# Performance work log

Measured on AMD Instinct MI355X. Metric: run time of the kernel, lower is better.

Reference implementation:

```python
import jax, jax.numpy as jnp
import numpy as np

BN_EPS = 1e-5


def _deconv_block(x, w, gamma, beta, mean, var):
    # Keras Conv2DTranspose(k=4, s=2, padding='valid') + Cropping2D(1) == pad (1,1) transpose conv: doubles H,W.
    y = jax.lax.conv_transpose(x, w, strides=(2, 2), padding=((1, 1), (1, 1)),
                               dimension_numbers=('NHWC', 'HWIO', 'NHWC'))
    # inference-mode BatchNorm followed by ReLU
    y = gamma * (y - mean) * jax.lax.rsqrt(var + BN_EPS) + beta
    return jax.nn.relu(y)


def _heatmap_max_det(hm):
    # hm: [B, H, W, K] (channels_last). Vectorized version of HeatmapMaxDetBlock.
    B, H, W, K = hm.shape
    flat = jnp.transpose(hm.reshape(B, H * W, K), (0, 2, 1))  # [B, K, HW]
    idx = jnp.argmax(flat, axis=2)                            # [B, K] int
    scores = jnp.max(flat, axis=2)                            # [B, K]
    pos = scores > 0.0                                        # scores_mask
    px = jnp.where(pos, (idx % W).astype(jnp.int32), 0)       # masked integer coords
    py = jnp.where(pos, (idx // W).astype(jnp.int32), 0)
    inner = (px > 0) & (px < W - 1) & (py > 0) & (py < H - 1)
    base = py * W + px

    def g(off):
        i = jnp.clip(base + off, 0, H * W - 1)                # clip keeps gathers in-bounds; masked by `inner`
        return jnp.take_along_axis(flat, i[..., None], axis=2)[..., 0]

    dx = jnp.where(inner, jnp.sign(g(1) - g(-1)) * 0.25, 0.0)   # subpixel refine in x
    dy = jnp.where(inner, jnp.sign(g(W) - g(-W)) * 0.25, 0.0)   # subpixel refine in y
    pts_x = px.astype(hm.dtype) + dx
    pts_y = py.astype(hm.dtype) + dy
    return jnp.stack([pts_x, pts_y, scores], axis=-1)            # [B, K, 3]


def setup_inputs() -> dict:
    key = jax.random.key(0)
    ks = jax.random.split(key, 24)
    B, Hf, Wf, Cb = 64, 8, 6, 2048
    C, KPT = 256, 17
    d = {}
    d['x'] = jax.random.normal(ks[0], (B, Hf, Wf, Cb), jnp.float32)
    ins = [Cb, C, C]
    for i in range(3):
        j = 1 + 6 * i
        d[f'w{i+1}'] = jax.random.normal(ks[j], (4, 4, ins[i], C), jnp.float32) * 0.05
        d[f'g{i+1}'] = jnp.ones((C,), jnp.float32) + 0.1 * jax.random.normal(ks[j + 1], (C,), jnp.float32)
        d[f'b{i+1}'] = 0.1 * jax.random.normal(ks[j + 2], (C,), jnp.float32)
        d[f'm{i+1}'] = 0.1 * jax.random.normal(ks[j + 3], (C,), jnp.float32)
        d[f'v{i+1}'] = 0.5 + jax.random.uniform(ks[j + 4], (C,), jnp.float32)
    d['wf'] = jax.random.normal(ks[20], (C, KPT), jnp.float32) * 0.05
    d['bf'] = 0.01 * jax.random.normal(ks[21], (KPT,), jnp.float32)
    return d


def reference(x, w1, g1, b1, m1, v1, w2, g2, b2, m2, v2, w3, g3, b3, m3, v3, wf, bf):
    y = _deconv_block(x, w1, g1, b1, m1, v1)   # [B,16,12,256]
    y = _deconv_block(y, w2, g2, b2, m2, v2)   # [B,32,24,256]
    y = _deconv_block(y, w3, g3, b3, m3, v3)   # [B,64,48,256]
    heatmap = jnp.einsum('bhwc,ck->bhwk', y, wf) + bf  # conv1x1 final block, [B,64,48,17]
    return _heatmap_max_det(heatmap)           # [B,17,3] (x, y, score)
```

## Files before the change

### kernel.cpp

```cpp
#include <hip/hip_runtime.h>


#define BN_EPS 1e-5f

typedef __attribute__((ext_vector_type(8))) short short8;
typedef __attribute__((ext_vector_type(4))) short short4v;
typedef __attribute__((ext_vector_type(4))) float float4v;
typedef unsigned int uint;

__device__ __forceinline__ float4v mfma16(short8 a, short8 b, float4v c) {
  return __builtin_amdgcn_mfma_f32_16x16x32_bf16(a, b, c, 0, 0, 0);
}

__device__ __forceinline__ void bf16split(float v, short& h, short& l) {
  const uint u  = __float_as_uint(v);
  const uint hb = (u + 0x7FFFu + ((u >> 16) & 1u)) >> 16;
  const float hf = __uint_as_float(hb << 16);
  const float lo = v - hf;
  const uint ul = __float_as_uint(lo);
  const uint lb = (ul + 0x7FFFu + ((ul >> 16) & 1u)) >> 16;
  h = (short)hb; l = (short)lb;
}

__device__ __forceinline__ uint pack2(short h0, short h1) {
  return (uint)(unsigned short)h0 | ((uint)(unsigned short)h1 << 16);
}

template <int CIN>
__global__ __launch_bounds__(256) void convert_w(
    const float* __restrict__ wg, short* __restrict__ wh, short* __restrict__ wl)
{
  constexpr int NCH = CIN / 32;
  __shared__ float tile[32][33];
  const int tap = blockIdx.x, ch = blockIdx.y, cb2 = blockIdx.z;
  const int tid = threadIdx.x;
#pragma unroll
  for (int k = 0; k < 4; ++k) {
    const int idx = k * 256 + tid;
    const int ci_l = idx >> 5, co_l = idx & 31;
    tile[ci_l][co_l] =
        wg[((size_t)(tap * CIN) + ch * 32 + ci_l) * 256 + cb2 * 32 + co_l];
  }
  __syncthreads();
#pragma unroll
  for (int k = 0; k < 2; ++k) {
    const int dd = k * 256 + tid;
    const int f = dd >> 8, wd = dd & 255;
    const int lane = wd >> 2, jp = (wd & 3) * 2;
    const int quad = lane >> 4, lrow = lane & 15;
    const int ci_l = quad * 8 + jp, co_l = f * 16 + lrow;
    short h0, l0, h1, l1;
    bf16split(tile[ci_l][co_l], h0, l0);
    bf16split(tile[ci_l + 1][co_l], h1, l1);
    const size_t off = ((size_t)((tap * NCH + ch) * 16 + cb2 * 2 + f)) * 512 +
                       lane * 8 + jp;
    *(uint*)(wh + off) = pack2(h0, h1);
    *(uint*)(wl + off) = pack2(l0, l1);
  }
}

__global__ __launch_bounds__(256) void convert_wf(
    const float* __restrict__ wf, short* __restrict__ wh, short* __restrict__ wl)
{
  const int b = blockIdx.x;
  const int ch = b >> 1, cb = b & 1;
  const int t = threadIdx.x;
  const int lane = t >> 2, jp = (t & 3) * 2;
  const int quad = lane >> 4, lrow = lane & 15;
  const int ci = ch * 32 + quad * 8 + jp;
  const int co = cb * 16 + lrow;
  const float v0 = (co < 17) ? wf[ci * 17 + co] : 0.f;
  const float v1 = (co < 17) ? wf[(ci + 1) * 17 + co] : 0.f;
  short h0, l0, h1, l1;
  bf16split(v0, h0, l0); bf16split(v1, h1, l1);
  const size_t off = (size_t)b * 512 + lane * 8 + jp;
  *(uint*)(wh + off) = pack2(h0, h1);
  *(uint*)(wl + off) = pack2(l0, l1);
}

template <int CIN, int H_IN, int W_IN, int MT, bool FUSE>
__global__ __launch_bounds__(256, 2) void deconv_mfma(
    const short* __restrict__ yh, const short* __restrict__ yl,
    const short* __restrict__ wbh, const short* __restrict__ wbl,
    const float* __restrict__ gg, const float* __restrict__ bg,
    const float* __restrict__ mg, const float* __restrict__ vg,
    float* __restrict__ og,
    short* __restrict__ oh_, short* __restrict__ ol_,
    const short* __restrict__ wfh, const short* __restrict__ wfl,
    const float* __restrict__ bfg)
{
  constexpr int R = H_IN - 1, C = W_IN - 1, NPIX = R * C;
  constexpr int H_OUT = 2 * H_IN - 2, W_OUT = 2 * W_IN - 2;
  constexpr int MF = MT / 16;
  constexpr int NCH = CIN / 32;
  constexpr int OUTSPAN = (MT + C - 2) / C + 1;
  constexpr int RSPAN = OUTSPAN + 1;
  constexpr int CIP = 40;
  constexpr int POS = RSPAN * W_IN;
  constexpr int AN = POS * CIP;
  constexpr int NITEM = POS * 16;
  constexpr int NIT = (NITEM + 255) / 256;
  constexpr int YSP = 264;

  __shared__ __align__(16) short ah_s[2][AN];
  __shared__ __align__(16) short al_s[2][AN];
  __shared__ __align__(16) short ysh_s[FUSE ? 32 * YSP : 1];
  __shared__ __align__(16) short ysl_s[FUSE ? 32 * YSP : 1];

  const int tid = threadIdx.x;
  const int wid = tid >> 6, lane = tid & 63;
  const int quad = lane >> 4, lrow = lane & 15;
  const int n0 = wid << 6;
  const int p = (int)(blockIdx.y >> 1), q = (int)(blockIdx.y & 1);
  const int n = blockIdx.z;

  int tapid[4];
#pragma unroll
  for (int t = 0; t < 4; ++t)
    tapid[t] = ((1 - p + 2 * (t >> 1)) << 2) + (1 - q + 2 * (t & 1));

  const int p0 = (int)blockIdx.x * MT;
  const int r_base = p0 / C;

  int abase[MF];
#pragma unroll
  for (int mf = 0; mf < MF; ++mf) {
    int pidx = p0 + mf * 16 + lrow;
    if (pidx > NPIX - 1) pidx = NPIX - 1;
    const int r = pidx / C, c = pidx % C;
    abase[mf] = ((r - r_base) * W_IN + c) * CIP + (quad << 3);
  }

  const int s_half = (tid >> 3) & 1;
  const short* __restrict__ gsrc = s_half ? yl : yh;
  int s_goff[NIT], s_loff[NIT];
#pragma unroll
  for (int k = 0; k < NIT; ++k) {
    const int i = k * 256 + tid;
    const int pos = i >> 4, sub = i & 7;
    const int row = pos / W_IN, col = pos - row * W_IN;
    int ih = r_base + row;
    if (ih > H_IN - 1) ih = H_IN - 1;
    s_goff[k] = ((n * H_IN + ih) * W_IN + col) * CIN + sub * 4;
    s_loff[k] = pos * CIP + sub * 4;
  }

  float4v acc[MF][4];
#pragma unroll
  for (int mf = 0; mf < MF; ++mf)
#pragma unroll
    for (int nf = 0; nf < 4; ++nf) acc[mf][nf] = (float4v){0.f, 0.f, 0.f, 0.f};

  short4v rv[NIT];
#pragma unroll
  for (int k = 0; k < NIT; ++k)
    if (NITEM % 256 == 0 || k * 256 + tid < NITEM)
      rv[k] = *(const short4v*)(gsrc + s_goff[k]);
  {
    short* lb = s_half ? &al_s[0][0] : &ah_s[0][0];
#pragma unroll
    for (int k = 0; k < NIT; ++k)
      if (NITEM % 256 == 0 || k * 256 + tid < NITEM)
        *(short4v*)(lb + s_loff[k]) = rv[k];
  }
  __syncthreads();

#pragma unroll 1
  for (int ck = 0; ck < NCH; ++ck) {
    const int b = ck & 1;
    const bool pre = (ck + 1 < NCH);
    if (pre) {
      const int ci0 = (ck + 1) * 32;
#pragma unroll
      for (int k = 0; k < NIT; ++k)
        if (NITEM % 256 == 0 || k * 256 + tid < NITEM)
          rv[k] = *(const short4v*)(gsrc + s_goff[k] + ci0);
    }
    const short* ab  = &ah_s[b][0];
    const short* alp = &al_s[b][0];
#pragma unroll
    for (int t = 0; t < 4; ++t) {
      short8 Bh[4], Bl[4];
#pragma unroll
      for (int nf = 0; nf < 4; ++nf) {
        const size_t fo =
            ((size_t)((tapid[t] * NCH + ck) * 16 + (wid << 2) + nf)) * 512 + lane * 8;
        Bh[nf] = *(const short8*)(wbh + fo);
        Bl[nf] = *(const short8*)(wbl + fo);
      }
      const int toff = ((t >> 1) * W_IN + (t & 1)) * CIP;
#pragma unroll
      for (int mf = 0; mf < MF; ++mf) {
        const short8 Ah = *(const short8*)(ab + abase[mf] + toff);
        const short8 Al = *(const short8*)(alp + abase[mf] + toff);
#pragma unroll
        for (int nf = 0; nf < 4; ++nf) {
          acc[mf][nf] = mfma16(Ah, Bh[nf], acc[mf][nf]);
          acc[mf][nf] = mfma16(Ah, Bl[nf], acc[mf][nf]);
          acc[mf][nf] = mfma16(Al, Bh[nf], acc[mf][nf]);
        }
      }
    }
    if (pre) {
      short* lb = s_half ? &al_s[b ^ 1][0] : &ah_s[b ^ 1][0];
#pragma unroll
      for (int k = 0; k < NIT; ++k)
        if (NITEM % 256 == 0 || k * 256 + tid < NITEM)
          *(short4v*)(lb + s_loff[k]) = rv[k];
    }
    __syncthreads();
  }

  float scv[4], shv[4];
#pragma unroll
  for (int nf = 0; nf < 4; ++nf) {
    const int co = n0 + nf * 16 + lrow;
    const float sc = gg[co] * rsqrtf(vg[co] + BN_EPS);
    scv[nf] = sc; shv[nf] = bg[co] - mg[co] * sc;
  }

  if constexpr (!FUSE) {
#pragma unroll
    for (int mf = 0; mf < MF; ++mf)
#pragma unroll
      for (int reg = 0; reg < 4; ++reg) {
        const int pidx = p0 + mf * 16 + (quad << 2) + reg;
        if (pidx < NPIX) {
          const int r = pidx / C, c = pidx % C;
          const int oh = 2 * r + p, ow = 2 * c + q;
          const size_t base =
              ((size_t)(n * H_OUT + oh) * W_OUT + ow) * 256 + n0 + lrow;
#pragma unroll
          for (int nf = 0; nf < 4; ++nf) {
            const float v = fmaxf(0.f, fmaf(acc[mf][nf][reg], scv[nf], shv[nf]));
            short h, l; bf16split(v, h, l);
            oh_[base + nf * 16] = h;
            ol_[base + nf * 16] = l;
          }
        }
      }
  } else {
    constexpr int NSUB = MT / 32;
    const int co_out = (wid << 4) + lrow;
#pragma unroll
    for (int s = 0; s < NSUB; ++s) {
      __syncthreads();
#pragma unroll
      for (int mh = 0; mh < 2; ++mh) {
        const int mf = 2 * s + mh;
        const int pl = (mh << 4) + (quad << 2);
#pragma unroll
        for (int reg = 0; reg < 4; ++reg)
#pragma unroll
          for (int nf = 0; nf < 4; ++nf) {
            const float v = fmaxf(0.f, fmaf(acc[mf][nf][reg], scv[nf], shv[nf]));
            short h, l; bf16split(v, h, l);
            const int o = (pl + reg) * YSP + n0 + nf * 16 + lrow;
            ysh_s[o] = h; ysl_s[o] = l;
          }
      }
      __syncthreads();
      if (wid < 2) {
        float4v hacc[2];
        hacc[0] = (float4v){0.f, 0.f, 0.f, 0.f};
        hacc[1] = (float4v){0.f, 0.f, 0.f, 0.f};
#pragma unroll
        for (int ch = 0; ch < 8; ++ch) {
          const size_t bo = (size_t)(ch * 2 + wid) * 512 + lane * 8;
          const short8 Hh = *(const short8*)(wfh + bo);
          const short8 Hl = *(const short8*)(wfl + bo);
#pragma unroll
          for (int mh = 0; mh < 2; ++mh) {
            const int yo = (mh * 16 + lrow) * YSP + (ch << 5) + (quad << 3);
            const short8 Ah = *(const short8*)(ysh_s + yo);
            const short8 Al = *(const short8*)(ysl_s + yo);
            hacc[mh] = mfma16(Ah, Hh, hacc[mh]);
            hacc[mh] = mfma16(Ah, Hl, hacc[mh]);
            hacc[mh] = mfma16(Al, Hh, hacc[mh]);
          }
        }
        if (co_out < 17) {
          const float bias = bfg[co_out];
#pragma unroll
          for (int mh = 0; mh < 2; ++mh)
#pragma unroll
            for (int reg = 0; reg < 4; ++reg) {
              const int pidx = p0 + s * 32 + mh * 16 + (quad << 2) + reg;
              if (pidx < NPIX) {
                const int r = pidx / C, c = pidx % C;
                const int oh = 2 * r + p, ow = 2 * c + q;
                og[((size_t)(n * H_OUT + oh) * W_OUT + ow) * 17 + co_out] =
                    hacc[mh][reg] + bias;
              }
            }
        }
      }
    }
  }
}

template <int MT, int KS>
__global__ __launch_bounds__(256, 2) void deconv1_mfma(
    const float* __restrict__ xg,
    const short* __restrict__ wbh, const short* __restrict__ wbl,
    float* __restrict__ og)
{
  constexpr int CIN = 2048, NCH = 64, H_IN = 8, W_IN = 6;
  constexpr int MF = MT / 16;
  constexpr int NSPAN = 5, CIP = 40;
  constexpr int NCK = CIN / 32 / KS;
  constexpr int POS = NSPAN * 48;
  constexpr int AN = POS * CIP;
  constexpr int NIT = POS * 16 / 256;

  __shared__ __align__(16) short ah_s[2][AN];
  __shared__ __align__(16) short al_s[2][AN];

  const int tid = threadIdx.x;
  const int wid = tid >> 6, lane = tid & 63;
  const int quad = lane >> 4, lrow = lane & 15;
  const int n0 = wid << 6;
  const int p = (int)(blockIdx.y >> 1), q = (int)(blockIdx.y & 1);
  const int ks = blockIdx.z;

  int tapid[4];
#pragma unroll
  for (int t = 0; t < 4; ++t)
    tapid[t] = ((1 - p + 2 * (t >> 1)) << 2) + (1 - q + 2 * (t & 1));

  const int m0 = (int)blockIdx.x * MT;
  const int n_base = m0 / 35;

  int abase[MF];
#pragma unroll
  for (int mf = 0; mf < MF; ++mf) {
    const int mg_ = m0 + mf * 16 + lrow;
    const int nl = mg_ / 35 - n_base;
    const int pix = mg_ % 35;
    const int r = pix / 5, c = pix % 5;
    abase[mf] = ((nl * H_IN + r) * W_IN + c) * CIP + (quad << 3);
  }

  const int tp = tid >> 4, cc2 = tid & 15;
  int goff[NIT];
#pragma unroll
  for (int k = 0; k < NIT; ++k) {
    const int pos = k * 16 + tp;
    const int nl = pos / 48, loc = pos - nl * 48;
    int ng = n_base + nl;
    if (ng > 63) ng = 63;
    goff[k] = (ng * 48 + loc) * CIN + cc2 * 2;
  }
  const int loff0 = tp * CIP + cc2 * 2;

  float4v acc[MF][4];
#pragma unroll
  for (int mf = 0; mf < MF; ++mf)
#pragma unroll
    for (int nf = 0; nf < 4; ++nf) acc[mf][nf] = (float4v){0.f, 0.f, 0.f, 0.f};

  const int cibase = ks * (CIN / KS);
  float2 rv[NIT];
#pragma unroll
  for (int k = 0; k < NIT; ++k)
    rv[k] = *(const float2*)(xg + goff[k] + cibase);
#pragma unroll
  for (int k = 0; k < NIT; ++k) {
    short h0, l0, h1, l1;
    bf16split(rv[k].x, h0, l0); bf16split(rv[k].y, h1, l1);
    const int o = loff0 + k * 16 * CIP;
    *(uint*)(&ah_s[0][0] + o) = pack2(h0, h1);
    *(uint*)(&al_s[0][0] + o) = pack2(l0, l1);
  }
  __syncthreads();

#pragma unroll 1
  for (int ck = 0; ck < NCK; ++ck) {
    const int b = ck & 1;
    const bool pre = (ck + 1 < NCK);
    if (pre) {
      const int ci0 = cibase + (ck + 1) * 32;
#pragma unroll
      for (int k = 0; k < NIT; ++k)
        rv[k] = *(const float2*)(xg + goff[k] + ci0);
    }
    const int ch = ks * NCK + ck;
    const short* ab  = &ah_s[b][0];
    const short* alp = &al_s[b][0];
#pragma unroll
    for (int t = 0; t < 4; ++t) {
      short8 Bh[4], Bl[4];
#pragma unroll
      for (int nf = 0; nf < 4; ++nf) {
        const size_t fo =
            ((size_t)((tapid[t] * NCH + ch) * 16 + (wid << 2) + nf)) * 512 + lane * 8;
        Bh[nf] = *(const short8*)(wbh + fo);
        Bl[nf] = *(const short8*)(wbl + fo);
      }
      const int toff = ((t >> 1) * W_IN + (t & 1)) * CIP;
#pragma unroll
      for (int mf = 0; mf < MF; ++mf) {
        const short8 Ah = *(const short8*)(ab + abase[mf] + toff);
        const short8 Al = *(const short8*)(alp + abase[mf] + toff);
#pragma unroll
        for (int nf = 0; nf < 4; ++nf) {
          acc[mf][nf] = mfma16(Ah, Bh[nf], acc[mf][nf]);
          acc[mf][nf] = mfma16(Ah, Bl[nf], acc[mf][nf]);
          acc[mf][nf] = mfma16(Al, Bh[nf], acc[mf][nf]);
        }
      }
    }
    if (pre) {
      short* hb = &ah_s[b ^ 1][0];
      short* lb = &al_s[b ^ 1][0];
#pragma unroll
      for (int k = 0; k < NIT; ++k) {
        short h0, l0, h1, l1;
        bf16split(rv[k].x, h0, l0); bf16split(rv[k].y, h1, l1);
        const int o = loff0 + k * 16 * CIP;
        *(uint*)(hb + o) = pack2(h0, h1);
        *(uint*)(lb + o) = pack2(l0, l1);
      }
    }
    __syncthreads();
  }

#pragma unroll
  for (int mf = 0; mf < MF; ++mf)
#pragma unroll
    for (int reg = 0; reg < 4; ++reg) {
      const int mg_ = m0 + mf * 16 + (quad << 2) + reg;
      const int nn = mg_ / 35, pix = mg_ % 35;
      const int r = pix / 5, c = pix % 5;
      const int oh = 2 * r + p, ow = 2 * c + q;
      float* dst = og + ((size_t)(nn * 14 + oh) * 10 + ow) * 256 + n0 + lrow;
#pragma unroll
      for (int nf = 0; nf < 4; ++nf)
        atomicAdd(dst + nf * 16, acc[mf][nf][reg]);
    }
}

__global__ __launch_bounds__(256) void bn1_split_kernel(
    const float* __restrict__ y, short* __restrict__ yh, short* __restrict__ yl,
    const float* __restrict__ gg, const float* __restrict__ bg,
    const float* __restrict__ mg, const float* __restrict__ vg, int nquad)
{
  for (int i = blockIdx.x * 256 + threadIdx.x; i < nquad; i += gridDim.x * 256) {
    const float4v x = *(const float4v*)(y + (size_t)i * 4);
    const int co0 = (i * 4) & 255;
    short4v hv, lv;
#pragma unroll
    for (int j = 0; j < 4; ++j) {
      const int co = co0 + j;
      const float sc = gg[co] * rsqrtf(vg[co] + BN_EPS);
      const float v = fmaxf(0.f, fmaf(x[j], sc, bg[co] - mg[co] * sc));
      short h, l; bf16split(v, h, l);
      hv[j] = h; lv[j] = l;
    }
    *(short4v*)(yh + (size_t)i * 4) = hv;
    *(short4v*)(yl + (size_t)i * 4) = lv;
  }
}

__global__ __launch_bounds__(256) void heatmap_det(const float* __restrict__ hm,
                                                   float* __restrict__ out)
{
  constexpr int H = 50, W = 34, HW = H * W, K = 17;
  const int b = blockIdx.x, k = blockIdx.y;
  const int tid = threadIdx.x;

  float best = -INFINITY;
  int bi = 0;
  for (int pos = tid; pos < HW; pos += 256) {
    const float v = hm[((size_t)b * HW + pos) * K + k];
    if (v > best) { best = v; bi = pos; }
  }
  __shared__ float sv[256];
  __shared__ int si[256];
  sv[tid] = best; si[tid] = bi;
  __syncthreads();
  for (int s = 128; s > 0; s >>= 1) {
    if (tid < s) {
      const float v2 = sv[tid + s]; const int i2 = si[tid + s];
      if (v2 > sv[tid] || (v2 == sv[tid] && i2 < si[tid])) { sv[tid] = v2; si[tid] = i2; }
    }
    __syncthreads();
  }
  if (tid == 0) {
    const float score = sv[0];
    const int idx = si[0];
    float ptx = 0.f, pty = 0.f;
    if (score > 0.f) {
      const int px = idx % W, py = idx / W;
      float dx = 0.f, dy = 0.f;
      if (px > 0 && px < W - 1 && py > 0 && py < H - 1) {
        auto g = [&](int off) {
          int i = idx + off;
          i = i < 0 ? 0 : (i > HW - 1 ? HW - 1 : i);
          return hm[((size_t)b * HW + i) * K + k];
        };
        const float d1 = g(1) - g(-1);
        const float d2 = g(W) - g(-W);
        dx = d1 > 0.f ? 0.25f : (d1 < 0.f ? -0.25f : 0.f);
        dy = d2 > 0.f ? 0.25f : (d2 < 0.f ? -0.25f : 0.f);
      }
      ptx = (float)px + dx;
      pty = (float)py + dy;
    }
    out[((size_t)b * K + k) * 3 + 0] = ptx;
    out[((size_t)b * K + k) * 3 + 1] = pty;
    out[((size_t)b * K + k) * 3 + 2] = score;
  }
}

extern "C" void kernel_launch(void* const* d_in, const int* in_sizes, int n_in,
                              void* d_out, int out_size, void* d_ws, size_t ws_size,
                              hipStream_t stream)
{
  const float* x  = (const float*)d_in[0];
  const float* w1 = (const float*)d_in[1];
  const float* g1 = (const float*)d_in[2];
  const float* b1 = (const float*)d_in[3];
  const float* m1 = (const float*)d_in[4];
  const float* v1 = (const float*)d_in[5];
  const float* w2 = (const float*)d_in[6];
  const float* g2 = (const float*)d_in[7];
  const float* b2 = (const float*)d_in[8];
  const float* m2 = (const float*)d_in[9];
  const float* v2 = (const float*)d_in[10];
  const float* w3 = (const float*)d_in[11];
  const float* g3 = (const float*)d_in[12];
  const float* b3 = (const float*)d_in[13];
  const float* m3 = (const float*)d_in[14];
  const float* v3 = (const float*)d_in[15];
  const float* wf = (const float*)d_in[16];
  const float* bf = (const float*)d_in[17];

  char* ws = (char*)d_ws;
  float* y1  = (float*)(ws + 0);
  short* w2h = (short*)(ws + 0);
  short* w2l = (short*)(ws + 2097152);
  float* hm  = (float*)(ws + 0);
  short* w1h = (short*)(ws + 9175040);
  short* w1l = (short*)(ws + 25952256);
  short* y1h = (short*)(ws + 9175040);
  short* y1l = (short*)(ws + 13762560);
  short* y2h = (short*)(ws + 18350080);
  short* y2l = (short*)(ws + 33685504);
  short* w3h = (short*)(ws + 49020928);
  short* w3l = (short*)(ws + 51118080);
  short* wfh = (short*)(ws + 53215232);
  short* wfl = (short*)(ws + 53231616);

  convert_w<2048><<<dim3(16, 64, 8), 256, 0, stream>>>(w1, w1h, w1l);
  convert_w<256><<<dim3(16, 8, 8), 256, 0, stream>>>(w3, w3h, w3l);
  convert_wf<<<dim3(16), 256, 0, stream>>>(wf, wfh, wfl);

  hipMemsetAsync(y1, 0, 9175040, stream);
  deconv1_mfma<112, 8><<<dim3(20, 4, 8), 256, 0, stream>>>(x, w1h, w1l, y1);
  bn1_split_kernel<<<dim3(1024), 256, 0, stream>>>(y1, y1h, y1l, g1, b1, m1, v1,
                                                   64 * 14 * 10 * 256 / 4);

  convert_w<256><<<dim3(16, 8, 8), 256, 0, stream>>>(w2, w2h, w2l);

  deconv_mfma<256, 14, 10, 64, false><<<dim3(2, 4, 64), 256, 0, stream>>>(
      y1h, y1l, w2h, w2l, g2, b2, m2, v2, nullptr, y2h, y2l,
      nullptr, nullptr, nullptr);

  deconv_mfma<256, 26, 18, 96, true><<<dim3(5, 4, 64), 256, 0, stream>>>(
      y2h, y2l, w3h, w3l, g3, b3, m3, v3, hm, nullptr, nullptr, wfh, wfl, bf);

  heatmap_det<<<dim3(64, 17), 256, 0, stream>>>(hm, (float*)d_out);
}
```

Before: 575.6 us.

## Single-buffer deconv1 LDS, shrink span, and remap grid so K-splits are adjacent

```diff
diff --git a/kernel.cpp b/kernel.cpp
--- a/kernel.cpp
+++ b/kernel.cpp
@@ -307,28 +307,33 @@
 {
   constexpr int CIN = 2048, NCH = 64, H_IN = 8, W_IN = 6;
   constexpr int MF = MT / 16;
-  constexpr int NSPAN = 5, CIP = 40;
+  constexpr int NSPAN = 4, CIP = 40;
   constexpr int NCK = CIN / 32 / KS;
   constexpr int POS = NSPAN * 48;
   constexpr int AN = POS * CIP;
   constexpr int NIT = POS * 16 / 256;
 
-  __shared__ __align__(16) short ah_s[2][AN];
-  __shared__ __align__(16) short al_s[2][AN];
+  __shared__ __align__(16) short ah_s[AN];
+  __shared__ __align__(16) short al_s[AN];
 
   const int tid = threadIdx.x;
   const int wid = tid >> 6, lane = tid & 63;
   const int quad = lane >> 4, lrow = lane & 15;
   const int n0 = wid << 6;
-  const int p = (int)(blockIdx.y >> 1), q = (int)(blockIdx.y & 1);
-  const int ks = blockIdx.z;
+
+  const int id = (int)blockIdx.x;
+  const int ks = id & 7;
+  const int slot = id >> 3;
+  const int tile = slot % 20;
+  const int py = slot / 20;
+  const int p = py >> 1, q = py & 1;
 
   int tapid[4];
 #pragma unroll
   for (int t = 0; t < 4; ++t)
     tapid[t] = ((1 - p + 2 * (t >> 1)) << 2) + (1 - q + 2 * (t & 1));
 
-  const int m0 = (int)blockIdx.x * MT;
+  const int m0 = tile * MT;
   const int n_base = m0 / 35;
 
   int abase[MF];
@@ -364,29 +369,26 @@
 #pragma unroll
   for (int k = 0; k < NIT; ++k)
     rv[k] = *(const float2*)(xg + goff[k] + cibase);
-#pragma unroll
-  for (int k = 0; k < NIT; ++k) {
-    short h0, l0, h1, l1;
-    bf16split(rv[k].x, h0, l0); bf16split(rv[k].y, h1, l1);
-    const int o = loff0 + k * 16 * CIP;
-    *(uint*)(&ah_s[0][0] + o) = pack2(h0, h1);
-    *(uint*)(&al_s[0][0] + o) = pack2(l0, l1);
-  }
-  __syncthreads();
 
 #pragma unroll 1
   for (int ck = 0; ck < NCK; ++ck) {
-    const int b = ck & 1;
-    const bool pre = (ck + 1 < NCK);
-    if (pre) {
+    __syncthreads();
+#pragma unroll
+    for (int k = 0; k < NIT; ++k) {
+      short h0, l0, h1, l1;
+      bf16split(rv[k].x, h0, l0); bf16split(rv[k].y, h1, l1);
+      const int o = loff0 + k * 16 * CIP;
+      *(uint*)(ah_s + o) = pack2(h0, h1);
+      *(uint*)(al_s + o) = pack2(l0, l1);
+    }
+    __syncthreads();
+    if (ck + 1 < NCK) {
       const int ci0 = cibase + (ck + 1) * 32;
 #pragma unroll
       for (int k = 0; k < NIT; ++k)
         rv[k] = *(const float2*)(xg + goff[k] + ci0);
     }
     const int ch = ks * NCK + ck;
-    const short* ab  = &ah_s[b][0];
-    const short* alp = &al_s[b][0];
 #pragma unroll
     for (int t = 0; t < 4; ++t) {
       short8 Bh[4], Bl[4];
@@ -400,8 +402,8 @@
       const int toff = ((t >> 1) * W_IN + (t & 1)) * CIP;
 #pragma unroll
       for (int mf = 0; mf < MF; ++mf) {
-        const short8 Ah = *(const short8*)(ab + abase[mf] + toff);
-        const short8 Al = *(const short8*)(alp + abase[mf] + toff);
+        const short8 Ah = *(const short8*)(ah_s + abase[mf] + toff);
+        const short8 Al = *(const short8*)(al_s + abase[mf] + toff);
 #pragma unroll
         for (int nf = 0; nf < 4; ++nf) {
           acc[mf][nf] = mfma16(Ah, Bh[nf], acc[mf][nf]);
@@ -410,19 +412,6 @@
         }
       }
     }
-    if (pre) {
-      short* hb = &ah_s[b ^ 1][0];
-      short* lb = &al_s[b ^ 1][0];
-#pragma unroll
-      for (int k = 0; k < NIT; ++k) {
-        short h0, l0, h1, l1;
-        bf16split(rv[k].x, h0, l0); bf16split(rv[k].y, h1, l1);
-        const int o = loff0 + k * 16 * CIP;
-        *(uint*)(hb + o) = pack2(h0, h1);
-        *(uint*)(lb + o) = pack2(l0, l1);
-      }
-    }
-    __syncthreads();
   }
 
 #pragma unroll
@@ -557,7 +546,7 @@
   convert_wf<<<dim3(16), 256, 0, stream>>>(wf, wfh, wfl);
 
   hipMemsetAsync(y1, 0, 9175040, stream);
-  deconv1_mfma<112, 8><<<dim3(20, 4, 8), 256, 0, stream>>>(x, w1h, w1l, y1);
+  deconv1_mfma<112, 8><<<dim3(640), 256, 0, stream>>>(x, w1h, w1l, y1);
   bn1_split_kernel<<<dim3(1024), 256, 0, stream>>>(y1, y1h, y1l, g1, b1, m1, v1,
                                                    64 * 14 * 10 * 256 / 4);
 
```

After: 541.3 us. 1.06x faster.
